# Optimization experiments

Hardware: AMD Instinct MI355X
Metric: run time of the kernel (lower is better)

## Reference

```python
import jax, jax.numpy as jnp
import numpy as np

B, H, W = 128, 64, 64
MAP = 128          # gff mapping_dim
GFF_SCALE = 10.0   # common default scale for Gaussian Fourier features


def _ku(k, shape, fan_in):
    # torch kaiming_uniform_(a=sqrt(5)) -> bound = 1/sqrt(fan_in)
    b = 1.0 / np.sqrt(fan_in)
    return jax.random.uniform(k, shape, jnp.float32, -b, b)


def setup_inputs() -> dict:
    key = jax.random.key(0)
    ks = jax.random.split(key, 16)
    coords = jax.random.uniform(ks[0], (B, 2, H, W), jnp.float32)
    Bmat = GFF_SCALE * jax.random.normal(ks[1], (2, MAP), jnp.float32)
    # FMMLinear(256, 256_out? no) -- linear1: in=256, out=256, rank=70
    L1 = _ku(ks[2], (256, 70), 70)
    R1 = _ku(ks[3], (70, 256), 256)
    b1 = jax.random.uniform(ks[4], (256,), jnp.float32, -1/np.sqrt(256), 1/np.sqrt(256))
    # linear2: in=256, out=128, rank=10
    L2 = _ku(ks[5], (128, 10), 10)
    R2 = _ku(ks[6], (10, 256), 256)
    b2 = jax.random.uniform(ks[7], (128,), jnp.float32, -1/np.sqrt(256), 1/np.sqrt(256))
    # dense layers (torch nn.Linear default init)
    W3 = _ku(ks[8], (32, 128), 128)
    b3 = jax.random.uniform(ks[9], (32,), jnp.float32, -1/np.sqrt(128), 1/np.sqrt(128))
    W4 = _ku(ks[10], (16, 32), 32)
    b4 = jax.random.uniform(ks[11], (16,), jnp.float32, -1/np.sqrt(32), 1/np.sqrt(32))
    W5 = _ku(ks[12], (3, 16), 16)
    b5 = jax.random.uniform(ks[13], (3,), jnp.float32, -1/np.sqrt(16), 1/np.sqrt(16))
    return dict(coords=coords, Bmat=Bmat, L1=L1, R1=R1, b1=b1,
                L2=L2, R2=R2, b2=b2, W3=W3, b3=b3, W4=W4, b4=b4, W5=W5, b5=b5)


def reference(coords, Bmat, L1, R1, b1, L2, R2, b2, W3, b3, W4, b4, W5, b5):
    # Gaussian Fourier features: [B,2,H,W] -> [B,H,W,2*MAP]
    proj = (2.0 * jnp.pi) * jnp.einsum('bchw,cm->bhwm', coords, Bmat)
    x = jnp.concatenate([jnp.sin(proj), jnp.cos(proj)], axis=-1)
    x = x.reshape(-1, 2 * MAP)                       # (b h w) c
    x = jax.nn.relu(x @ (L1 @ R1).T + b1)            # FMM linear1
    x = jax.nn.relu(x @ (L2 @ R2).T + b2)            # FMM linear2
    x = jax.nn.relu(x @ W3.T + b3)
    x = jax.nn.relu(x @ W4.T + b4)
    out = (x @ W5.T + b5)[None]                      # [1, B*H*W, 3]
    return out
```

## Files before the change

### kernel.cpp

```cpp
#include <hip/hip_runtime.h>


typedef __attribute__((ext_vector_type(8))) short bf16x8;
typedef __attribute__((ext_vector_type(4))) float f32x4;
typedef __attribute__((ext_vector_type(4))) int i32x4;

#define LFENCE() asm volatile("s_waitcnt lgkmcnt(0)" ::: "memory")

__device__ inline unsigned short f2bf(float f) {
  unsigned u = __float_as_uint(f);
  return (unsigned short)((u + 0x7FFFu + ((u >> 16) & 1u)) >> 16);
}

#if __has_builtin(__builtin_amdgcn_cvt_pk_bf16_f32)
typedef __attribute__((ext_vector_type(2))) __bf16 bf16x2;
__device__ inline unsigned pk2bf(float a, float b) {
  bf16x2 v = __builtin_amdgcn_cvt_pk_bf16_f32(a, b);
  return __builtin_bit_cast(unsigned, v);
}
#else
__device__ inline unsigned pk2bf(float a, float b) {
  return ((__float_as_uint(a) + 0x8000u) >> 16) |
         ((__float_as_uint(b) + 0x8000u) & 0xFFFF0000u);
}
#endif

__global__ __launch_bounds__(256) void prep_pack(
    const float* __restrict__ R1, const float* __restrict__ L1,
    const float* __restrict__ R2, const float* __restrict__ L2,
    const float* __restrict__ W3, const float* __restrict__ W4,
    const float* __restrict__ b1, const float* __restrict__ b2,
    void* __restrict__ ws) {
  unsigned short* w16 = (unsigned short*)ws;
  int e = blockIdx.x * 256 + threadIdx.x;
  if (e < 20480) {
    int kt = e / 2560, rem = e % 2560;
    int n = rem >> 5, oj = rem & 31;
    int k = kt * 32 + oj;
    int feat = (k & 1) ? 128 + (k >> 1) : (k >> 1);
    w16[e] = f2bf((n < 70) ? R1[n * 256 + feat] : 0.0f);
  } else if (e < 45056) {
    int f = e - 20480;
    int kt = f / 8192, rem = f % 8192;
    int n = rem >> 5, oj = rem & 31;
    int r = kt * 32 + (oj & 1) * 16 + (oj >> 1);
    float v = (r < 70) ? L1[n * 70 + r] : (r == 80 ? b1[n] : 0.0f);
    w16[e] = f2bf(v);
  } else if (e < 49152) {
    int g = e - 45056;
    int rd = g / 512, rem = g % 512;
    int n = rem >> 5, oj = rem & 31;
    int j = rd * 32 + (oj & 1) * 16 + (oj >> 1);
    w16[e] = f2bf((n < 10) ? R2[n * 256 + j] : 0.0f);
  } else if (e < 53248) {
    int f = e - 49152;
    int k = f & 31, n = (f >> 5) & 15, nt = f >> 9;
    int i = nt * 16 + n;
    float v = (k < 10) ? L2[i * 10 + k] : (k == 10 ? b2[i] : 0.0f);
    w16[e] = f2bf(v);
  } else if (e < 57344) {
    int f = e - 53248;
    int oj = f & 31, n = (f >> 5) & 15, s = (f >> 9) & 1, rd = f >> 10;
    int i = rd * 32 + (oj & 1) * 16 + (oj >> 1);
    w16[e] = f2bf(W3[(s * 16 + n) * 128 + i]);
  } else if (e < 57856) {
    int f = e - 57344;
    int n = f >> 5, oj = f & 31;
    int q = (oj & 1) * 16 + (oj >> 1);
    w16[e] = f2bf(W4[n * 32 + q]);
  }
}

__global__ __launch_bounds__(64, 2) void mlp_mfma(
    const float* __restrict__ coords, const float* __restrict__ Bm,
    const float* __restrict__ b3v, const float* __restrict__ b4v,
    const float* __restrict__ W5, const float* __restrict__ b5,
    const void* __restrict__ ws, float* __restrict__ out) {
  const int l = threadIdx.x;
  const int lo = l & 15, hi = l >> 4;
  const int pix0 = blockIdx.x * 64;

  __shared__ __align__(16) char smem[13312];
  unsigned short* Y16 = (unsigned short*)smem;
  unsigned short* X16 = (unsigned short*)smem;
  float* O4f = (float*)smem;

  const unsigned short* R1p = (const unsigned short*)ws;
  const unsigned short* L1p = ((const unsigned short*)ws) + 20480;
  const unsigned short* R2p = ((const unsigned short*)ws) + 45056;
  const unsigned short* L2p = ((const unsigned short*)ws) + 49152;
  const unsigned short* W3p = ((const unsigned short*)ws) + 53248;
  const unsigned short* W4p = ((const unsigned short*)ws) + 57344;

  const f32x4 fz = {0.0f, 0.0f, 0.0f, 0.0f};

  float c0m[4], c1m[4];
#pragma unroll
  for (int mt = 0; mt < 4; ++mt) {
    int p = pix0 + mt * 16 + lo;
    int bb = p >> 12, hw = p & 4095;
    c0m[mt] = coords[bb * 8192 + hw];
    c1m[mt] = coords[bb * 8192 + 4096 + hw];
  }

  f32x4 y[4][5];
#pragma unroll
  for (int mt = 0; mt < 4; ++mt)
#pragma unroll
    for (int nt = 0; nt < 5; ++nt) y[mt][nt] = fz;

#pragma unroll
  for (int kt = 0; kt < 8; ++kt) {
    bf16x8 bfr[5];
#pragma unroll
    for (int nt = 0; nt < 5; ++nt)
      bfr[nt] = *(const bf16x8*)(R1p + (kt * 80 + nt * 16 + lo) * 32 + hi * 8);
    bf16x8 af[4];
#pragma unroll
    for (int mt = 0; mt < 4; ++mt) {
#pragma unroll
      for (int p = 0; p < 4; ++p) {
        int m = kt * 16 + hi * 4 + p;
        float u = fmaf(c0m[mt], Bm[m], c1m[mt] * Bm[128 + m]);
        float t = __builtin_amdgcn_fractf(u);
        float s = __builtin_amdgcn_sinf(t);
        float c = __builtin_amdgcn_cosf(t);
        ((unsigned*)&af[mt])[p] = pk2bf(s, c);
      }
    }
#pragma unroll
    for (int mt = 0; mt < 4; ++mt)
#pragma unroll
      for (int nt = 0; nt < 5; ++nt)
        y[mt][nt] = __builtin_amdgcn_mfma_f32_16x16x32_bf16(af[mt], bfr[nt],
                                                            y[mt][nt], 0, 0, 0);
  }

#pragma unroll
  for (int mt = 0; mt < 4; ++mt)
#pragma unroll
    for (int r = 0; r < 4; ++r) {
      int row = mt * 16 + hi * 4 + r;
      *(unsigned*)(Y16 + row * 104 + lo * 2)      = pk2bf(y[mt][0][r], y[mt][1][r]);
      *(unsigned*)(Y16 + row * 104 + 32 + lo * 2) = pk2bf(y[mt][2][r], y[mt][3][r]);
      *(unsigned*)(Y16 + row * 104 + 64 + lo * 2) = pk2bf(y[mt][4][r], 0.0f);
    }
  Y16[l * 104 + 65] = 0x3F80;

  bf16x8 WE[3], WO[3], WEn[3], WOn[3];
#pragma unroll
  for (int kt = 0; kt < 3; ++kt) {
    WE[kt] = *(const bf16x8*)(L1p + (kt * 256 + lo) * 32 + hi * 8);
    WO[kt] = *(const bf16x8*)(L1p + (kt * 256 + 16 + lo) * 32 + hi * 8);
  }
  bf16x8 br_c = *(const bf16x8*)(R2p + lo * 32 + hi * 8);
  bf16x8 br_u, br_n;

  LFENCE();
  bf16x8 ay[4][3];
#pragma unroll
  for (int mt = 0; mt < 4; ++mt)
#pragma unroll
    for (int kt = 0; kt < 3; ++kt)
      ay[mt][kt] = *(const bf16x8*)(Y16 + (mt * 16 + lo) * 104 + kt * 32 + hi * 8);

  f32x4 zfr[4];
#pragma unroll
  for (int mt = 0; mt < 4; ++mt) zfr[mt] = fz;
  bf16x8 aa[4];

#pragma unroll
  for (int rd = 0; rd <= 8; ++rd) {
    f32x4 cfE[4], cfO[4];
    if (rd < 8) {
#pragma unroll
      for (int mt = 0; mt < 4; ++mt) { cfE[mt] = fz; cfO[mt] = fz; }
#pragma unroll
      for (int kt = 0; kt < 3; ++kt)
#pragma unroll
        for (int mt = 0; mt < 4; ++mt) {
          cfE[mt] = __builtin_amdgcn_mfma_f32_16x16x32_bf16(ay[mt][kt], WE[kt],
                                                            cfE[mt], 0, 0, 0);
          cfO[mt] = __builtin_amdgcn_mfma_f32_16x16x32_bf16(ay[mt][kt], WO[kt],
                                                            cfO[mt], 0, 0, 0);
        }
    }
    if (rd > 0) {
#pragma unroll
      for (int mt = 0; mt < 4; ++mt)
        zfr[mt] = __builtin_amdgcn_mfma_f32_16x16x32_bf16(aa[mt], br_u,
                                                          zfr[mt], 0, 0, 0);
    }
    if (rd < 8) {
      unsigned short* Xb = X16 + (rd & 1) * 2560;
#pragma unroll
      for (int mt = 0; mt < 4; ++mt)
#pragma unroll
        for (int r = 0; r < 4; ++r) {
          float v0 = fmaxf(cfE[mt][r], 0.0f);
          float v1 = fmaxf(cfO[mt][r], 0.0f);
          *(unsigned*)(Xb + (mt * 16 + hi * 4 + r) * 40 + lo * 2) = pk2bf(v0, v1);
        }
      if (rd < 7) {
#pragma unroll
        for (int kt = 0; kt < 3; ++kt) {
          WEn[kt] = *(const bf16x8*)(L1p + (kt * 256 + (2 * rd + 2) * 16 + lo) * 32 + hi * 8);
          WOn[kt] = *(const bf16x8*)(L1p + (kt * 256 + (2 * rd + 3) * 16 + lo) * 32 + hi * 8);
        }
        br_n = *(const bf16x8*)(R2p + ((rd + 1) * 16 + lo) * 32 + hi * 8);
      }
      LFENCE();
#pragma unroll
      for (int mt = 0; mt < 4; ++mt)
        aa[mt] = *(const bf16x8*)(Xb + (mt * 16 + lo) * 40 + hi * 8);
      br_u = br_c; br_c = br_n;
#pragma unroll
      for (int kt = 0; kt < 3; ++kt) { WE[kt] = WEn[kt]; WO[kt] = WOn[kt]; }
    }
  }

  unsigned short* Z16 = X16;
#pragma unroll
  for (int mt = 0; mt < 4; ++mt)
#pragma unroll
    for (int r = 0; r < 4; ++r)
      Z16[(mt * 16 + hi * 4 + r) * 40 + lo] =
          (unsigned short)(pk2bf(zfr[mt][r], 0.0f) & 0xFFFFu);
  *(i32x4*)(Z16 + l * 40 + 16) = (i32x4){0, 0, 0, 0};
  *(i32x4*)(Z16 + l * 40 + 24) = (i32x4){0, 0, 0, 0};
  Z16[l * 40 + 10] = 0x3F80;

  bf16x8 wlE = *(const bf16x8*)(L2p + lo * 32 + hi * 8);
  bf16x8 wlO = *(const bf16x8*)(L2p + (16 + lo) * 32 + hi * 8);
  bf16x8 wlEn, wlOn;
  bf16x8 bw_c0 = *(const bf16x8*)(W3p + lo * 32 + hi * 8);
  bf16x8 bw_c1 = *(const bf16x8*)(W3p + (16 + lo) * 32 + hi * 8);
  bf16x8 bw_u0, bw_u1, bw_n0, bw_n1;

  LFENCE();
  bf16x8 az[4];
#pragma unroll
  for (int mt = 0; mt < 4; ++mt)
    az[mt] = *(const bf16x8*)(Z16 + (mt * 16 + lo) * 40 + hi * 8);

  f32x4 o3fr[4][2];
#pragma unroll
  for (int mt = 0; mt < 4; ++mt) { o3fr[mt][0] = fz; o3fr[mt][1] = fz; }
  bf16x8 aaC[4];

#pragma unroll
  for (int rd = 0; rd <= 4; ++rd) {
    f32x4 cfE[4], cfO[4];
    if (rd < 4) {
#pragma unroll
      for (int mt = 0; mt < 4; ++mt) {
        cfE[mt] = __builtin_amdgcn_mfma_f32_16x16x32_bf16(az[mt], wlE, fz, 0, 0, 0);
        cfO[mt] = __builtin_amdgcn_mfma_f32_16x16x32_bf16(az[mt], wlO, fz, 0, 0, 0);
      }
    }
    if (rd > 0) {
#pragma unroll
      for (int mt = 0; mt < 4; ++mt) {
        o3fr[mt][0] = __builtin_amdgcn_mfma_f32_16x16x32_bf16(aaC[mt], bw_u0,
                                                              o3fr[mt][0], 0, 0, 0);
        o3fr[mt][1] = __builtin_amdgcn_mfma_f32_16x16x32_bf16(aaC[mt], bw_u1,
                                                              o3fr[mt][1], 0, 0, 0);
      }
    }
    if (rd < 4) {
      unsigned short* Xb = X16 + (rd & 1) * 2560;
#pragma unroll
      for (int mt = 0; mt < 4; ++mt)
#pragma unroll
        for (int r = 0; r < 4; ++r) {
          float v0 = fmaxf(cfE[mt][r], 0.0f);
          float v1 = fmaxf(cfO[mt][r], 0.0f);
          *(unsigned*)(Xb + (mt * 16 + hi * 4 + r) * 40 + lo * 2) = pk2bf(v0, v1);
        }
      if (rd < 3) {
        wlEn = *(const bf16x8*)(L2p + ((2 * rd + 2) * 16 + lo) * 32 + hi * 8);
        wlOn = *(const bf16x8*)(L2p + ((2 * rd + 3) * 16 + lo) * 32 + hi * 8);
        bw_n0 = *(const bf16x8*)(W3p + ((2 * rd + 2) * 16 + lo) * 32 + hi * 8);
        bw_n1 = *(const bf16x8*)(W3p + ((2 * rd + 3) * 16 + lo) * 32 + hi * 8);
      }
      LFENCE();
#pragma unroll
      for (int mt = 0; mt < 4; ++mt)
        aaC[mt] = *(const bf16x8*)(Xb + (mt * 16 + lo) * 40 + hi * 8);
      bw_u0 = bw_c0; bw_u1 = bw_c1; bw_c0 = bw_n0; bw_c1 = bw_n1;
      wlE = wlEn; wlO = wlOn;
    }
  }

  float b3E = b3v[lo], b3O = b3v[16 + lo];
  unsigned short* Db = X16;
#pragma unroll
  for (int mt = 0; mt < 4; ++mt)
#pragma unroll
    for (int r = 0; r < 4; ++r) {
      float v0 = fmaxf(o3fr[mt][0][r] + b3E, 0.0f);
      float v1 = fmaxf(o3fr[mt][1][r] + b3O, 0.0f);
      *(unsigned*)(Db + (mt * 16 + hi * 4 + r) * 40 + lo * 2) = pk2bf(v0, v1);
    }
  bf16x8 bw4 = *(const bf16x8*)(W4p + lo * 32 + hi * 8);
  float b4l = b4v[lo];
  LFENCE();
  bf16x8 aD[4];
#pragma unroll
  for (int mt = 0; mt < 4; ++mt)
    aD[mt] = *(const bf16x8*)(Db + (mt * 16 + lo) * 40 + hi * 8);
  f32x4 o4fr[4];
#pragma unroll
  for (int mt = 0; mt < 4; ++mt)
    o4fr[mt] = __builtin_amdgcn_mfma_f32_16x16x32_bf16(aD[mt], bw4, fz, 0, 0, 0);

#pragma unroll
  for (int mt = 0; mt < 4; ++mt)
#pragma unroll
    for (int r = 0; r < 4; ++r)
      O4f[(mt * 16 + hi * 4 + r) * 17 + lo] = fmaxf(o4fr[mt][r] + b4l, 0.0f);
  LFENCE();
  float o4l[16];
#pragma unroll
  for (int q = 0; q < 16; ++q) o4l[q] = O4f[l * 17 + q];

#pragma unroll
  for (int e = 0; e < 3; ++e) {
    float acc = b5[e];
    const float* __restrict__ w5 = W5 + e * 16;
#pragma unroll
    for (int p = 0; p < 16; ++p) acc = fmaf(o4l[p], w5[p], acc);
    out[(pix0 + l) * 3 + e] = acc;
  }
}

extern "C" void kernel_launch(void* const* d_in, const int* in_sizes, int n_in,
                              void* d_out, int out_size, void* d_ws, size_t ws_size,
                              hipStream_t stream) {
  const float* coords = (const float*)d_in[0];
  const float* Bmat   = (const float*)d_in[1];
  const float* L1     = (const float*)d_in[2];
  const float* R1     = (const float*)d_in[3];
  const float* b1     = (const float*)d_in[4];
  const float* L2     = (const float*)d_in[5];
  const float* R2     = (const float*)d_in[6];
  const float* b2     = (const float*)d_in[7];
  const float* W3     = (const float*)d_in[8];
  const float* b3     = (const float*)d_in[9];
  const float* W4     = (const float*)d_in[10];
  const float* b4     = (const float*)d_in[11];
  const float* W5     = (const float*)d_in[12];
  const float* b5     = (const float*)d_in[13];

  prep_pack<<<227, 256, 0, stream>>>(R1, L1, R2, L2, W3, W4, b1, b2, d_ws);
  mlp_mfma<<<8192, 64, 0, stream>>>(coords, Bmat, b3, b4, W5, b5,
                                    d_ws, (float*)d_out);
}
```

Before: 156.0 us.

## Process 128 pixels per wavefront to amortize weight-fragment loads

Each single-wave block now handles 128 pixels (8 M-tiles) instead of 64, and the grid is halved. Every weight fragment loaded from global memory (L1, R2, L2, W3) now feeds twice as many MFMAs, which cuts weight traffic per pixel. In exchange the software-pipelined prefetch of next-round weights is dropped in favour of loads inside each round. LDS per block doubles and more register state is live (ay[8][3], zfr[8], o3A/o3B), which risks lower occupancy or spills.

Measured after the change: 196.9 us. 26.2% more time.

```diff
diff --git a/kernel.cpp b/kernel.cpp
--- a/kernel.cpp
+++ b/kernel.cpp
@@ -78,9 +78,9 @@
     const void* __restrict__ ws, float* __restrict__ out) {
   const int l = threadIdx.x;
   const int lo = l & 15, hi = l >> 4;
-  const int pix0 = blockIdx.x * 64;
-
-  __shared__ __align__(16) char smem[13312];
+  const int pix0 = blockIdx.x * 128;
+
+  __shared__ __align__(16) char smem[26624];
   unsigned short* Y16 = (unsigned short*)smem;
   unsigned short* X16 = (unsigned short*)smem;
   float* O4f = (float*)smem;
@@ -94,243 +94,218 @@
 
   const f32x4 fz = {0.0f, 0.0f, 0.0f, 0.0f};
 
-  float c0m[4], c1m[4];
-#pragma unroll
-  for (int mt = 0; mt < 4; ++mt) {
+  float c0m[8], c1m[8];
+#pragma unroll
+  for (int mt = 0; mt < 8; ++mt) {
     int p = pix0 + mt * 16 + lo;
     int bb = p >> 12, hw = p & 4095;
     c0m[mt] = coords[bb * 8192 + hw];
     c1m[mt] = coords[bb * 8192 + 4096 + hw];
   }
 
-  f32x4 y[4][5];
-#pragma unroll
-  for (int mt = 0; mt < 4; ++mt)
-#pragma unroll
-    for (int nt = 0; nt < 5; ++nt) y[mt][nt] = fz;
-
-#pragma unroll
-  for (int kt = 0; kt < 8; ++kt) {
-    bf16x8 bfr[5];
-#pragma unroll
-    for (int nt = 0; nt < 5; ++nt)
-      bfr[nt] = *(const bf16x8*)(R1p + (kt * 80 + nt * 16 + lo) * 32 + hi * 8);
-    bf16x8 af[4];
-#pragma unroll
-    for (int mt = 0; mt < 4; ++mt) {
-#pragma unroll
-      for (int p = 0; p < 4; ++p) {
-        int m = kt * 16 + hi * 4 + p;
-        float u = fmaf(c0m[mt], Bm[m], c1m[mt] * Bm[128 + m]);
-        float t = __builtin_amdgcn_fractf(u);
-        float s = __builtin_amdgcn_sinf(t);
-        float c = __builtin_amdgcn_cosf(t);
-        ((unsigned*)&af[mt])[p] = pk2bf(s, c);
+#pragma unroll
+  for (int ps = 0; ps < 2; ++ps) {
+    f32x4 y[4][5];
+#pragma unroll
+    for (int mtl = 0; mtl < 4; ++mtl)
+#pragma unroll
+      for (int nt = 0; nt < 5; ++nt) y[mtl][nt] = fz;
+
+#pragma unroll
+    for (int kt = 0; kt < 8; ++kt) {
+      bf16x8 bfr[5];
+#pragma unroll
+      for (int nt = 0; nt < 5; ++nt)
+        bfr[nt] = *(const bf16x8*)(R1p + (kt * 80 + nt * 16 + lo) * 32 + hi * 8);
+      bf16x8 af[4];
+#pragma unroll
+      for (int mtl = 0; mtl < 4; ++mtl) {
+#pragma unroll
+        for (int p = 0; p < 4; ++p) {
+          int m = kt * 16 + hi * 4 + p;
+          float u = fmaf(c0m[ps * 4 + mtl], Bm[m],
+                         c1m[ps * 4 + mtl] * Bm[128 + m]);
+          float t = __builtin_amdgcn_fractf(u);
+          float s = __builtin_amdgcn_sinf(t);
+          float c = __builtin_amdgcn_cosf(t);
+          ((unsigned*)&af[mtl])[p] = pk2bf(s, c);
+        }
       }
-    }
-#pragma unroll
-    for (int mt = 0; mt < 4; ++mt)
-#pragma unroll
-      for (int nt = 0; nt < 5; ++nt)
-        y[mt][nt] = __builtin_amdgcn_mfma_f32_16x16x32_bf16(af[mt], bfr[nt],
-                                                            y[mt][nt], 0, 0, 0);
-  }
-
-#pragma unroll
-  for (int mt = 0; mt < 4; ++mt)
-#pragma unroll
-    for (int r = 0; r < 4; ++r) {
-      int row = mt * 16 + hi * 4 + r;
-      *(unsigned*)(Y16 + row * 104 + lo * 2)      = pk2bf(y[mt][0][r], y[mt][1][r]);
-      *(unsigned*)(Y16 + row * 104 + 32 + lo * 2) = pk2bf(y[mt][2][r], y[mt][3][r]);
-      *(unsigned*)(Y16 + row * 104 + 64 + lo * 2) = pk2bf(y[mt][4][r], 0.0f);
-    }
+#pragma unroll
+      for (int mtl = 0; mtl < 4; ++mtl)
+#pragma unroll
+        for (int nt = 0; nt < 5; ++nt)
+          y[mtl][nt] = __builtin_amdgcn_mfma_f32_16x16x32_bf16(af[mtl], bfr[nt],
+                                                               y[mtl][nt], 0, 0, 0);
+    }
+#pragma unroll
+    for (int mtl = 0; mtl < 4; ++mtl)
+#pragma unroll
+      for (int r = 0; r < 4; ++r) {
+        int row = ps * 64 + mtl * 16 + hi * 4 + r;
+        *(unsigned*)(Y16 + row * 104 + lo * 2)      = pk2bf(y[mtl][0][r], y[mtl][1][r]);
+        *(unsigned*)(Y16 + row * 104 + 32 + lo * 2) = pk2bf(y[mtl][2][r], y[mtl][3][r]);
+        *(unsigned*)(Y16 + row * 104 + 64 + lo * 2) = pk2bf(y[mtl][4][r], 0.0f);
+      }
+  }
   Y16[l * 104 + 65] = 0x3F80;
-
-  bf16x8 WE[3], WO[3], WEn[3], WOn[3];
-#pragma unroll
-  for (int kt = 0; kt < 3; ++kt) {
-    WE[kt] = *(const bf16x8*)(L1p + (kt * 256 + lo) * 32 + hi * 8);
-    WO[kt] = *(const bf16x8*)(L1p + (kt * 256 + 16 + lo) * 32 + hi * 8);
-  }
-  bf16x8 br_c = *(const bf16x8*)(R2p + lo * 32 + hi * 8);
-  bf16x8 br_u, br_n;
+  Y16[(64 + l) * 104 + 65] = 0x3F80;
 
   LFENCE();
-  bf16x8 ay[4][3];
-#pragma unroll
-  for (int mt = 0; mt < 4; ++mt)
+  bf16x8 ay[8][3];
+#pragma unroll
+  for (int mt = 0; mt < 8; ++mt)
 #pragma unroll
     for (int kt = 0; kt < 3; ++kt)
       ay[mt][kt] = *(const bf16x8*)(Y16 + (mt * 16 + lo) * 104 + kt * 32 + hi * 8);
 
-  f32x4 zfr[4];
-#pragma unroll
-  for (int mt = 0; mt < 4; ++mt) zfr[mt] = fz;
-  bf16x8 aa[4];
-
-#pragma unroll
-  for (int rd = 0; rd <= 8; ++rd) {
-    f32x4 cfE[4], cfO[4];
-    if (rd < 8) {
-#pragma unroll
-      for (int mt = 0; mt < 4; ++mt) { cfE[mt] = fz; cfO[mt] = fz; }
+  f32x4 zfr[8];
+#pragma unroll
+  for (int mt = 0; mt < 8; ++mt) zfr[mt] = fz;
+
+#pragma unroll
+  for (int rd = 0; rd < 8; ++rd) {
+    unsigned short* Xb = X16 + (rd & 1) * 5120;
+    bf16x8 WE[3], WO[3];
+#pragma unroll
+    for (int kt = 0; kt < 3; ++kt) {
+      WE[kt] = *(const bf16x8*)(L1p + (kt * 256 + (2 * rd) * 16 + lo) * 32 + hi * 8);
+      WO[kt] = *(const bf16x8*)(L1p + (kt * 256 + (2 * rd + 1) * 16 + lo) * 32 + hi * 8);
+    }
+#pragma unroll
+    for (int h = 0; h < 2; ++h) {
+      f32x4 cfE[4], cfO[4];
+#pragma unroll
+      for (int mtl = 0; mtl < 4; ++mtl) { cfE[mtl] = fz; cfO[mtl] = fz; }
 #pragma unroll
       for (int kt = 0; kt < 3; ++kt)
 #pragma unroll
-        for (int mt = 0; mt < 4; ++mt) {
-          cfE[mt] = __builtin_amdgcn_mfma_f32_16x16x32_bf16(ay[mt][kt], WE[kt],
-                                                            cfE[mt], 0, 0, 0);
-          cfO[mt] = __builtin_amdgcn_mfma_f32_16x16x32_bf16(ay[mt][kt], WO[kt],
-                                                            cfO[mt], 0, 0, 0);
+        for (int mtl = 0; mtl < 4; ++mtl) {
+          cfE[mtl] = __builtin_amdgcn_mfma_f32_16x16x32_bf16(
+              ay[h * 4 + mtl][kt], WE[kt], cfE[mtl], 0, 0, 0);
+          cfO[mtl] = __builtin_amdgcn_mfma_f32_16x16x32_bf16(
+              ay[h * 4 + mtl][kt], WO[kt], cfO[mtl], 0, 0, 0);
         }
-    }
-    if (rd > 0) {
-#pragma unroll
-      for (int mt = 0; mt < 4; ++mt)
-        zfr[mt] = __builtin_amdgcn_mfma_f32_16x16x32_bf16(aa[mt], br_u,
-                                                          zfr[mt], 0, 0, 0);
-    }
-    if (rd < 8) {
-      unsigned short* Xb = X16 + (rd & 1) * 2560;
-#pragma unroll
-      for (int mt = 0; mt < 4; ++mt)
+#pragma unroll
+      for (int mtl = 0; mtl < 4; ++mtl)
 #pragma unroll
         for (int r = 0; r < 4; ++r) {
-          float v0 = fmaxf(cfE[mt][r], 0.0f);
-          float v1 = fmaxf(cfO[mt][r], 0.0f);
-          *(unsigned*)(Xb + (mt * 16 + hi * 4 + r) * 40 + lo * 2) = pk2bf(v0, v1);
+          int row = (h * 4 + mtl) * 16 + hi * 4 + r;
+          float v0 = fmaxf(cfE[mtl][r], 0.0f);
+          float v1 = fmaxf(cfO[mtl][r], 0.0f);
+          *(unsigned*)(Xb + row * 40 + lo * 2) = pk2bf(v0, v1);
         }
-      if (rd < 7) {
-#pragma unroll
-        for (int kt = 0; kt < 3; ++kt) {
-          WEn[kt] = *(const bf16x8*)(L1p + (kt * 256 + (2 * rd + 2) * 16 + lo) * 32 + hi * 8);
-          WOn[kt] = *(const bf16x8*)(L1p + (kt * 256 + (2 * rd + 3) * 16 + lo) * 32 + hi * 8);
-        }
-        br_n = *(const bf16x8*)(R2p + ((rd + 1) * 16 + lo) * 32 + hi * 8);
-      }
-      LFENCE();
-#pragma unroll
-      for (int mt = 0; mt < 4; ++mt)
-        aa[mt] = *(const bf16x8*)(Xb + (mt * 16 + lo) * 40 + hi * 8);
-      br_u = br_c; br_c = br_n;
-#pragma unroll
-      for (int kt = 0; kt < 3; ++kt) { WE[kt] = WEn[kt]; WO[kt] = WOn[kt]; }
+    }
+    bf16x8 br = *(const bf16x8*)(R2p + (rd * 16 + lo) * 32 + hi * 8);
+    LFENCE();
+#pragma unroll
+    for (int mt = 0; mt < 8; ++mt) {
+      bf16x8 aa = *(const bf16x8*)(Xb + (mt * 16 + lo) * 40 + hi * 8);
+      zfr[mt] = __builtin_amdgcn_mfma_f32_16x16x32_bf16(aa, br, zfr[mt], 0, 0, 0);
     }
   }
 
   unsigned short* Z16 = X16;
 #pragma unroll
-  for (int mt = 0; mt < 4; ++mt)
+  for (int mt = 0; mt < 8; ++mt)
 #pragma unroll
     for (int r = 0; r < 4; ++r)
       Z16[(mt * 16 + hi * 4 + r) * 40 + lo] =
           (unsigned short)(pk2bf(zfr[mt][r], 0.0f) & 0xFFFFu);
-  *(i32x4*)(Z16 + l * 40 + 16) = (i32x4){0, 0, 0, 0};
-  *(i32x4*)(Z16 + l * 40 + 24) = (i32x4){0, 0, 0, 0};
-  Z16[l * 40 + 10] = 0x3F80;
-
-  bf16x8 wlE = *(const bf16x8*)(L2p + lo * 32 + hi * 8);
-  bf16x8 wlO = *(const bf16x8*)(L2p + (16 + lo) * 32 + hi * 8);
-  bf16x8 wlEn, wlOn;
-  bf16x8 bw_c0 = *(const bf16x8*)(W3p + lo * 32 + hi * 8);
-  bf16x8 bw_c1 = *(const bf16x8*)(W3p + (16 + lo) * 32 + hi * 8);
-  bf16x8 bw_u0, bw_u1, bw_n0, bw_n1;
-
+#pragma unroll
+  for (int t = 0; t < 2; ++t) {
+    int row = t * 64 + l;
+    *(i32x4*)(Z16 + row * 40 + 16) = (i32x4){0, 0, 0, 0};
+    *(i32x4*)(Z16 + row * 40 + 24) = (i32x4){0, 0, 0, 0};
+    Z16[row * 40 + 10] = 0x3F80;
+  }
   LFENCE();
-  bf16x8 az[4];
-#pragma unroll
-  for (int mt = 0; mt < 4; ++mt)
+  bf16x8 az[8];
+#pragma unroll
+  for (int mt = 0; mt < 8; ++mt)
     az[mt] = *(const bf16x8*)(Z16 + (mt * 16 + lo) * 40 + hi * 8);
 
-  f32x4 o3fr[4][2];
-#pragma unroll
-  for (int mt = 0; mt < 4; ++mt) { o3fr[mt][0] = fz; o3fr[mt][1] = fz; }
-  bf16x8 aaC[4];
-
-#pragma unroll
-  for (int rd = 0; rd <= 4; ++rd) {
-    f32x4 cfE[4], cfO[4];
-    if (rd < 4) {
-#pragma unroll
-      for (int mt = 0; mt < 4; ++mt) {
-        cfE[mt] = __builtin_amdgcn_mfma_f32_16x16x32_bf16(az[mt], wlE, fz, 0, 0, 0);
-        cfO[mt] = __builtin_amdgcn_mfma_f32_16x16x32_bf16(az[mt], wlO, fz, 0, 0, 0);
+  f32x4 o3A[8], o3B[8];
+#pragma unroll
+  for (int mt = 0; mt < 8; ++mt) { o3A[mt] = fz; o3B[mt] = fz; }
+
+#pragma unroll
+  for (int rd = 0; rd < 4; ++rd) {
+    unsigned short* Xb = X16 + (rd & 1) * 5120;
+    bf16x8 wlE = *(const bf16x8*)(L2p + ((2 * rd) * 16 + lo) * 32 + hi * 8);
+    bf16x8 wlO = *(const bf16x8*)(L2p + ((2 * rd + 1) * 16 + lo) * 32 + hi * 8);
+#pragma unroll
+    for (int h = 0; h < 2; ++h) {
+      f32x4 cfE[4], cfO[4];
+#pragma unroll
+      for (int mtl = 0; mtl < 4; ++mtl) {
+        cfE[mtl] = __builtin_amdgcn_mfma_f32_16x16x32_bf16(az[h * 4 + mtl], wlE,
+                                                           fz, 0, 0, 0);
+        cfO[mtl] = __builtin_amdgcn_mfma_f32_16x16x32_bf16(az[h * 4 + mtl], wlO,
+                                                           fz, 0, 0, 0);
       }
-    }
-    if (rd > 0) {
-#pragma unroll
-      for (int mt = 0; mt < 4; ++mt) {
-        o3fr[mt][0] = __builtin_amdgcn_mfma_f32_16x16x32_bf16(aaC[mt], bw_u0,
-                                                              o3fr[mt][0], 0, 0, 0);
-        o3fr[mt][1] = __builtin_amdgcn_mfma_f32_16x16x32_bf16(aaC[mt], bw_u1,
-                                                              o3fr[mt][1], 0, 0, 0);
-      }
-    }
-    if (rd < 4) {
-      unsigned short* Xb = X16 + (rd & 1) * 2560;
-#pragma unroll
-      for (int mt = 0; mt < 4; ++mt)
+#pragma unroll
+      for (int mtl = 0; mtl < 4; ++mtl)
 #pragma unroll
         for (int r = 0; r < 4; ++r) {
-          float v0 = fmaxf(cfE[mt][r], 0.0f);
-          float v1 = fmaxf(cfO[mt][r], 0.0f);
-          *(unsigned*)(Xb + (mt * 16 + hi * 4 + r) * 40 + lo * 2) = pk2bf(v0, v1);
+          int row = (h * 4 + mtl) * 16 + hi * 4 + r;
+          float v0 = fmaxf(cfE[mtl][r], 0.0f);
+          float v1 = fmaxf(cfO[mtl][r], 0.0f);
+          *(unsigned*)(Xb + row * 40 + lo * 2) = pk2bf(v0, v1);
         }
-      if (rd < 3) {
-        wlEn = *(const bf16x8*)(L2p + ((2 * rd + 2) * 16 + lo) * 32 + hi * 8);
-        wlOn = *(const bf16x8*)(L2p + ((2 * rd + 3) * 16 + lo) * 32 + hi * 8);
-        bw_n0 = *(const bf16x8*)(W3p + ((2 * rd + 2) * 16 + lo) * 32 + hi * 8);
-        bw_n1 = *(const bf16x8*)(W3p + ((2 * rd + 3) * 16 + lo) * 32 + hi * 8);
-      }
-      LFENCE();
-#pragma unroll
-      for (int mt = 0; mt < 4; ++mt)
-        aaC[mt] = *(const bf16x8*)(Xb + (mt * 16 + lo) * 40 + hi * 8);
-      bw_u0 = bw_c0; bw_u1 = bw_c1; bw_c0 = bw_n0; bw_c1 = bw_n1;
-      wlE = wlEn; wlO = wlOn;
+    }
+    bf16x8 bw0 = *(const bf16x8*)(W3p + ((rd * 2 + 0) * 16 + lo) * 32 + hi * 8);
+    bf16x8 bw1 = *(const bf16x8*)(W3p + ((rd * 2 + 1) * 16 + lo) * 32 + hi * 8);
+    LFENCE();
+#pragma unroll
+    for (int mt = 0; mt < 8; ++mt) {
+      bf16x8 aaC = *(const bf16x8*)(Xb + (mt * 16 + lo) * 40 + hi * 8);
+      o3A[mt] = __builtin_amdgcn_mfma_f32_16x16x32_bf16(aaC, bw0, o3A[mt], 0, 0, 0);
+      o3B[mt] = __builtin_amdgcn_mfma_f32_16x16x32_bf16(aaC, bw1, o3B[mt], 0, 0, 0);
     }
   }
 
   float b3E = b3v[lo], b3O = b3v[16 + lo];
   unsigned short* Db = X16;
 #pragma unroll
-  for (int mt = 0; mt < 4; ++mt)
+  for (int mt = 0; mt < 8; ++mt)
 #pragma unroll
     for (int r = 0; r < 4; ++r) {
-      float v0 = fmaxf(o3fr[mt][0][r] + b3E, 0.0f);
-      float v1 = fmaxf(o3fr[mt][1][r] + b3O, 0.0f);
-      *(unsigned*)(Db + (mt * 16 + hi * 4 + r) * 40 + lo * 2) = pk2bf(v0, v1);
+      int row = mt * 16 + hi * 4 + r;
+      float v0 = fmaxf(o3A[mt][r] + b3E, 0.0f);
+      float v1 = fmaxf(o3B[mt][r] + b3O, 0.0f);
+      *(unsigned*)(Db + row * 40 + lo * 2) = pk2bf(v0, v1);
     }
   bf16x8 bw4 = *(const bf16x8*)(W4p + lo * 32 + hi * 8);
   float b4l = b4v[lo];
   LFENCE();
-  bf16x8 aD[4];
-#pragma unroll
-  for (int mt = 0; mt < 4; ++mt)
-    aD[mt] = *(const bf16x8*)(Db + (mt * 16 + lo) * 40 + hi * 8);
-  f32x4 o4fr[4];
-#pragma unroll
-  for (int mt = 0; mt < 4; ++mt)
-    o4fr[mt] = __builtin_amdgcn_mfma_f32_16x16x32_bf16(aD[mt], bw4, fz, 0, 0, 0);
-
-#pragma unroll
-  for (int mt = 0; mt < 4; ++mt)
+  f32x4 o4fr[8];
+#pragma unroll
+  for (int mt = 0; mt < 8; ++mt) {
+    bf16x8 aD = *(const bf16x8*)(Db + (mt * 16 + lo) * 40 + hi * 8);
+    o4fr[mt] = __builtin_amdgcn_mfma_f32_16x16x32_bf16(aD, bw4, fz, 0, 0, 0);
+  }
+
+#pragma unroll
+  for (int mt = 0; mt < 8; ++mt)
 #pragma unroll
     for (int r = 0; r < 4; ++r)
       O4f[(mt * 16 + hi * 4 + r) * 17 + lo] = fmaxf(o4fr[mt][r] + b4l, 0.0f);
   LFENCE();
-  float o4l[16];
-#pragma unroll
-  for (int q = 0; q < 16; ++q) o4l[q] = O4f[l * 17 + q];
-
-#pragma unroll
-  for (int e = 0; e < 3; ++e) {
-    float acc = b5[e];
-    const float* __restrict__ w5 = W5 + e * 16;
-#pragma unroll
-    for (int p = 0; p < 16; ++p) acc = fmaf(o4l[p], w5[p], acc);
-    out[(pix0 + l) * 3 + e] = acc;
+
+#pragma unroll
+  for (int t = 0; t < 2; ++t) {
+    float o4l[16];
+#pragma unroll
+    for (int q = 0; q < 16; ++q) o4l[q] = O4f[(t * 64 + l) * 17 + q];
+#pragma unroll
+    for (int e = 0; e < 3; ++e) {
+      float acc = b5[e];
+      const float* __restrict__ w5 = W5 + e * 16;
+#pragma unroll
+      for (int p = 0; p < 16; ++p) acc = fmaf(o4l[p], w5[p], acc);
+      out[(pix0 + t * 64 + l) * 3 + e] = acc;
+    }
   }
 }
 
@@ -353,6 +328,6 @@
   const float* b5     = (const float*)d_in[13];
 
   prep_pack<<<227, 256, 0, stream>>>(R1, L1, R2, L2, W3, W4, b1, b2, d_ws);
-  mlp_mfma<<<8192, 64, 0, stream>>>(coords, Bmat, b3, b4, W5, b5,
+  mlp_mfma<<<4096, 64, 0, stream>>>(coords, Bmat, b3, b4, W5, b5,
                                     d_ws, (float*)d_out);
 }
```
